# Optimization experiments

Measured on AMD Instinct MI355X. Metric: run time of the kernel, lower is better.

The kernel has to match this reference:

```python
import jax, jax.numpy as jnp
import numpy as np
from jax import lax


def conv2d(x, w, b=None, pad=0, groups=1):
    y = lax.conv_general_dilated(x, w, (1, 1), [(pad, pad), (pad, pad)],
                                 dimension_numbers=('NCHW', 'OIHW', 'NCHW'),
                                 feature_group_count=groups)
    if b is not None:
        y = y + b[None, :, None, None]
    return y


def prelu(x, a):
    return jnp.where(x > 0, x, a * x)


def box_blur(x, k, p):
    # depthwise uniform box filter, groups=3, 'same' output size
    w = jnp.full((3, 1, k, k), 1.0 / (k * k), x.dtype)
    return conv2d(x, w, pad=p, groups=3)


def head(body, hw, hb, c1, c2):
    h = conv2d(body, hw, hb, pad=1)                      # [B,4,H,W]
    g = jnp.mean(h, axis=(2, 3), keepdims=True)          # CALayer: GAP
    s = jax.nn.sigmoid(conv2d(jax.nn.relu(conv2d(g, c1, pad=0)), c2, pad=0))
    return jax.nn.softmax(h * s, axis=1)                 # Softmax2d over channels


def fuse(x, h):
    # kernel_1 is a 1x1 identity conv -> just x
    m2 = box_blur(x, 5, 2)
    m3 = box_blur(x, 15, 7)
    m4 = box_blur(x, 25, 12)
    return h[:, 0:1] * x + h[:, 1:2] * m2 + h[:, 2:3] * m3 + h[:, 3:4] * m4


def setup_inputs() -> dict:
    key = jax.random.key(0)
    ks = jax.random.split(key, 20)
    f32 = jnp.float32
    d = {}
    d['x'] = jax.random.normal(ks[0], (8, 3, 512, 512), f32)
    # body convs
    d['bw1'] = jax.random.normal(ks[1], (32, 3, 3, 3), f32) * 0.05
    d['bb1'] = jnp.zeros((32,), f32)
    d['a1'] = jnp.full((1,), 0.25, f32)
    d['bw2'] = jax.random.normal(ks[2], (64, 32, 3, 3), f32) * 0.05
    d['bb2'] = jnp.zeros((64,), f32)
    d['a2'] = jnp.full((1,), 0.25, f32)
    d['bw3'] = jax.random.normal(ks[3], (32, 64, 3, 3), f32) * 0.05
    d['bb3'] = jnp.zeros((32,), f32)
    d['a3'] = jnp.full((1,), 0.25, f32)
    for i, k0 in zip((1, 2, 3), (4, 8, 12)):
        d[f'h{i}w'] = jax.random.normal(ks[k0], (4, 32, 3, 3), f32) * 0.05
        d[f'h{i}b'] = jnp.zeros((4,), f32)
        d[f'h{i}c1'] = jax.random.normal(ks[k0 + 1], (4, 4, 1, 1), f32) * 0.1
        d[f'h{i}c2'] = jax.random.normal(ks[k0 + 2], (4, 4, 1, 1), f32) * 0.1
    return d


def reference(x, bw1, bb1, a1, bw2, bb2, a2, bw3, bb3, a3,
              h1w, h1b, h1c1, h1c2,
              h2w, h2b, h2c1, h2c2,
              h3w, h3b, h3c1, h3c2):
    body = prelu(conv2d(x, bw1, bb1, pad=1), a1)
    body = prelu(conv2d(body, bw2, bb2, pad=1), a2)
    body = prelu(conv2d(body, bw3, bb3, pad=1), a3)
    h1 = head(body, h1w, h1b, h1c1, h1c2)
    h2 = head(body, h2w, h2b, h2c1, h2c2)
    h3 = head(body, h3w, h3b, h3c1, h3c2)
    out1 = fuse(x, h1)
    out2 = fuse(out1, h2)
    out3 = fuse(out2, h3)
    return out3
```

## Files before the change

### kernel.cpp

```cpp
#include <hip/hip_runtime.h>
#include <math.h>

#define HWSZ (512*512)

typedef unsigned int u32;
typedef __attribute__((ext_vector_type(8))) short short8;
typedef __attribute__((ext_vector_type(4))) float f32x4;

__device__ __forceinline__ unsigned short f2bf(float f) {
    unsigned u = __float_as_uint(f);
    unsigned r = (u + 0x7FFFu + ((u >> 16) & 1u)) >> 16;
    return (unsigned short)r;
}
__device__ __forceinline__ float bf2f(unsigned short h) {
    return __uint_as_float((unsigned)h << 16);
}
__device__ __forceinline__ u32 packhl(float v) {
    unsigned short h = f2bf(v);
    unsigned short l = f2bf(v - bf2f(h));
    return (u32)h | ((u32)l << 16);
}

#define GRAN  3464
#define APLANE (4 * GRAN)

__global__ void prep_weights(const float* __restrict__ w2, const float* __restrict__ w3,
                             const float* __restrict__ hw1, const float* __restrict__ hw2,
                             const float* __restrict__ hw3,
                             const float* __restrict__ hb1, const float* __restrict__ hb2,
                             const float* __restrict__ hb3,
                             unsigned short* __restrict__ w2h, unsigned short* __restrict__ w2l,
                             unsigned short* __restrict__ w3h, unsigned short* __restrict__ w3l,
                             unsigned short* __restrict__ whh, unsigned short* __restrict__ whl,
                             float* __restrict__ hb16)
{
    int i = blockIdx.x * 256 + threadIdx.x;
    if (i < 18432) {
        int tap = i / 2048, r = i % 2048, co = r / 32, ci = r % 32;
        float v = w2[((co * 32 + ci) * 9) + tap];
        unsigned short h = f2bf(v);
        w2h[i] = h; w2l[i] = f2bf(v - bf2f(h));
    } else if (i < 36864) {
        int e = i - 18432;
        int tap = e / 2048, r = e % 2048, co = r / 64, ci = r % 64;
        float v = w3[((co * 64 + ci) * 9) + tap];
        unsigned short h = f2bf(v);
        w3h[e] = h; w3l[e] = f2bf(v - bf2f(h));
    } else if (i < 41472) {
        int e = i - 36864;
        int tap = e / 512, r = e % 512, co16 = r / 32, ci = r % 32;
        float v = 0.f;
        if (co16 < 12) {
            int hd = co16 >> 2, cl = co16 & 3;
            const float* wp = hd == 0 ? hw1 : (hd == 1 ? hw2 : hw3);
            v = wp[((cl * 32 + ci) * 9) + tap];
        }
        unsigned short h = f2bf(v);
        whh[e] = h; whl[e] = f2bf(v - bf2f(h));
    } else if (i < 41488) {
        int j = i - 41472;
        float v = 0.f;
        if (j < 12) {
            const float* bp = (j >> 2) == 0 ? hb1 : ((j >> 2) == 1 ? hb2 : hb3);
            v = bp[j & 3];
        }
        hb16[j] = v;
    }
}

template<int CIN>
__device__ __forceinline__ void stage_tile(const u32* __restrict__ in,
                                           unsigned short* s_a,
                                           int w, int lane, int x1, int y0, int c0)
{
    const int c16 = lane & 15;
    const int g   = lane >> 4;
    for (int it = w; it < 30; it += 4) {
        int r  = it / 5;
        int cb = it % 5;
        int col = cb * 16 + c16;
        if (col < 66) {
            int gy = y0 - 1 + r;
            int gx = x1 - 1 + col;
            u32 d0=0,d1=0,d2=0,d3=0,d4=0,d5=0,d6=0,d7=0;
            if ((unsigned)gy < 512u && (unsigned)gx < 512u) {
                const uint4* p = (const uint4*)(in + ((size_t)(gy * 512 + gx)) * CIN + c0 + g * 8);
                uint4 A = p[0], B = p[1];
                d0=A.x; d1=A.y; d2=A.z; d3=A.w; d4=B.x; d5=B.y; d6=B.z; d7=B.w;
            }
            uint4 hi, lo;
            hi.x = (d0 & 0xffffu) | (d1 << 16);
            hi.y = (d2 & 0xffffu) | (d3 << 16);
            hi.z = (d4 & 0xffffu) | (d5 << 16);
            hi.w = (d6 & 0xffffu) | (d7 << 16);
            lo.x = (d0 >> 16) | (d1 & 0xffff0000u);
            lo.y = (d2 >> 16) | (d3 & 0xffff0000u);
            lo.z = (d4 >> 16) | (d5 & 0xffff0000u);
            lo.w = (d6 >> 16) | (d7 & 0xffff0000u);
            int e = (r * 72 + col) * 8;
            *(uint4*)(s_a + g * GRAN + e) = hi;
            *(uint4*)(s_a + APLANE + g * GRAN + e) = lo;
        }
    }
}

template<int CIN, int COUT>
__global__ __launch_bounds__(256, 2)
void conv_mfma(const u32* __restrict__ in,
               const unsigned short* __restrict__ wh,
               const unsigned short* __restrict__ wl,
               const float* __restrict__ bias,
               const float* __restrict__ alpha,
               u32* __restrict__ out)
{
    constexpr int NTW = COUT / 16;
    __shared__ __align__(16) unsigned short s_a[2 * APLANE];

    const int tid  = threadIdx.x;
    const int w    = tid >> 6;
    const int lane = tid & 63;
    const int ln   = lane & 15;
    const int quad = lane >> 4;
    const int x1   = blockIdx.x * 64;
    const int y0   = blockIdx.y * 4;

    f32x4 acc[4][NTW];
    #pragma unroll
    for (int mt = 0; mt < 4; ++mt)
        #pragma unroll
        for (int nt = 0; nt < NTW; ++nt)
            acc[mt][nt] = (f32x4){0.f, 0.f, 0.f, 0.f};

    for (int c0 = 0; c0 < CIN; c0 += 32) {
        if (c0) __syncthreads();
        stage_tile<CIN>(in, s_a, w, lane, x1, y0, c0);
        __syncthreads();

        #pragma unroll
        for (int tap = 0; tap < 9; ++tap) {
            const int dy = tap / 3, dx = tap % 3;
            short8 bh[NTW], bl[NTW];
            #pragma unroll
            for (int nt = 0; nt < NTW; ++nt) {
                size_t off = ((size_t)(tap * COUT + nt * 16 + ln)) * CIN + c0 + quad * 8;
                bh[nt] = *(const short8*)(wh + off);
                bl[nt] = *(const short8*)(wl + off);
            }
            short8 ah[4], al[4];
            #pragma unroll
            for (int mt = 0; mt < 4; ++mt) {
                const int mti = w * 4 + mt;
                const int rr  = (mti >> 2) + dy;
                const int col = ((mti & 3) << 4) + ln + dx;
                const int off = quad * GRAN + (rr * 72 + col) * 8;
                ah[mt] = *(const short8*)(s_a + off);
                al[mt] = *(const short8*)(s_a + APLANE + off);
            }
            #pragma unroll
            for (int mt = 0; mt < 4; ++mt)
                #pragma unroll
                for (int nt = 0; nt < NTW; ++nt)
                    acc[mt][nt] = __builtin_amdgcn_mfma_f32_16x16x32_bf16(ah[mt], bh[nt], acc[mt][nt], 0, 0, 0);
            #pragma unroll
            for (int mt = 0; mt < 4; ++mt)
                #pragma unroll
                for (int nt = 0; nt < NTW; ++nt)
                    acc[mt][nt] = __builtin_amdgcn_mfma_f32_16x16x32_bf16(al[mt], bh[nt], acc[mt][nt], 0, 0, 0);
            #pragma unroll
            for (int mt = 0; mt < 4; ++mt)
                #pragma unroll
                for (int nt = 0; nt < NTW; ++nt)
                    acc[mt][nt] = __builtin_amdgcn_mfma_f32_16x16x32_bf16(ah[mt], bl[nt], acc[mt][nt], 0, 0, 0);
        }
    }

    const float av = alpha[0];
    float bs[NTW];
    #pragma unroll
    for (int nt = 0; nt < NTW; ++nt) bs[nt] = bias[nt * 16 + ln];
    #pragma unroll
    for (int mt = 0; mt < 4; ++mt) {
        const int mti = w * 4 + mt;
        const int y   = y0 + (mti >> 2);
        const int xb  = x1 + ((mti & 3) << 4) + quad * 4;
        #pragma unroll
        for (int nt = 0; nt < NTW; ++nt) {
            const int co = nt * 16 + ln;
            #pragma unroll
            for (int reg = 0; reg < 4; ++reg) {
                float t = acc[mt][nt][reg] + bs[nt];
                t = t > 0.f ? t : av * t;
                out[((size_t)(y * 512 + xb + reg)) * COUT + co] = packhl(t);
            }
        }
    }
}

__global__ __launch_bounds__(256, 2)
void head_mfma(const u32* __restrict__ in,
               const unsigned short* __restrict__ wh,
               const unsigned short* __restrict__ wl,
               const float* __restrict__ hb,
               float* __restrict__ h, float* __restrict__ g2, int b)
{
    __shared__ __align__(16) unsigned short s_a[2 * APLANE];
    __shared__ float s_red[4][16];

    const int tid  = threadIdx.x;
    const int w    = tid >> 6;
    const int lane = tid & 63;
    const int ln   = lane & 15;
    const int quad = lane >> 4;
    const int x1   = blockIdx.x * 64;
    const int y0   = blockIdx.y * 4;

    f32x4 acc[4];
    #pragma unroll
    for (int mt = 0; mt < 4; ++mt) acc[mt] = (f32x4){0.f, 0.f, 0.f, 0.f};

    stage_tile<32>(in, s_a, w, lane, x1, y0, 0);
    __syncthreads();

    #pragma unroll
    for (int tap = 0; tap < 9; ++tap) {
        const int dy = tap / 3, dx = tap % 3;
        size_t boff = (size_t)tap * 512 + ln * 32 + quad * 8;
        short8 bh = *(const short8*)(wh + boff);
        short8 bl = *(const short8*)(wl + boff);
        short8 ah[4], al[4];
        #pragma unroll
        for (int mt = 0; mt < 4; ++mt) {
            const int mti = w * 4 + mt;
            const int rr  = (mti >> 2) + dy;
            const int col = ((mti & 3) << 4) + ln + dx;
            const int off = quad * GRAN + (rr * 72 + col) * 8;
            ah[mt] = *(const short8*)(s_a + off);
            al[mt] = *(const short8*)(s_a + APLANE + off);
        }
        #pragma unroll
        for (int mt = 0; mt < 4; ++mt)
            acc[mt] = __builtin_amdgcn_mfma_f32_16x16x32_bf16(ah[mt], bh, acc[mt], 0, 0, 0);
        #pragma unroll
        for (int mt = 0; mt < 4; ++mt)
            acc[mt] = __builtin_amdgcn_mfma_f32_16x16x32_bf16(al[mt], bh, acc[mt], 0, 0, 0);
        #pragma unroll
        for (int mt = 0; mt < 4; ++mt)
            acc[mt] = __builtin_amdgcn_mfma_f32_16x16x32_bf16(ah[mt], bl, acc[mt], 0, 0, 0);
    }

    __syncthreads();
    float* s_h = (float*)s_a;
    const float bs = hb[ln];
    float psum = 0.f;
    #pragma unroll
    for (int mt = 0; mt < 4; ++mt) {
        const int mti  = w * 4 + mt;
        const int base = (mti >> 2) * 64 + ((mti & 3) << 4) + quad * 4;
        #pragma unroll
        for (int reg = 0; reg < 4; ++reg) {
            float v = acc[mt][reg] + bs;
            if (ln < 12) s_h[ln * 260 + base + reg] = v;
            psum += v;
        }
    }
    psum += __shfl_down(psum, 16);
    psum += __shfl_down(psum, 32);
    if (lane < 16) s_red[w][lane] = psum;
    __syncthreads();

    if (tid < 192) {
        const int co = tid >> 4, ch = tid & 15;
        const float* src = s_h + co * 260 + ch * 16;
        float4 v0 = *(const float4*)(src);
        float4 v1 = *(const float4*)(src + 4);
        float4 v2 = *(const float4*)(src + 8);
        float4 v3 = *(const float4*)(src + 12);
        const int hd = co >> 2, cl = co & 3;
        float* dst = h + ((size_t)((hd * 8 + b) * 4 + cl)) * HWSZ
                       + (size_t)(y0 + (ch >> 2)) * 512 + x1 + ((ch & 3) << 4);
        *(float4*)(dst)      = v0;
        *(float4*)(dst + 4)  = v1;
        *(float4*)(dst + 8)  = v2;
        *(float4*)(dst + 12) = v3;
    }
    if (tid < 12) {
        float t = s_red[0][tid] + s_red[1][tid] + s_red[2][tid] + s_red[3][tid];
        atomicAdd(&g2[(tid >> 2) * 32 + b * 4 + (tid & 3)], t);
    }
}

__global__ __launch_bounds__(256)
void conv1_nhwc(const float* __restrict__ x, const float* __restrict__ wgt,
                const float* __restrict__ bias, const float* __restrict__ alpha,
                u32* __restrict__ out)
{
    __shared__ float s_in[3][6][72];
    __shared__ float s_w[3][9][32];
    __shared__ float s_b[32];
    const int tid = threadIdx.x;
    const int x1 = blockIdx.x * 64, y0 = blockIdx.y * 4;

    for (int i = tid; i < 3 * 6 * 66; i += 256) {
        int ci = i / 396, rm = i % 396;
        int r = rm / 66, cc = rm % 66;
        int gy = y0 - 1 + r, gx = x1 - 1 + cc;
        float v = 0.f;
        if ((unsigned)gy < 512u && (unsigned)gx < 512u)
            v = x[(size_t)ci * HWSZ + gy * 512 + gx];
        s_in[ci][r][cc] = v;
    }
    for (int i = tid; i < 864; i += 256) {
        int co = i & 31, rm = i >> 5;
        int ci = rm / 9, tap = rm % 9;
        s_w[ci][tap][co] = wgt[(co * 3 + ci) * 9 + tap];
    }
    if (tid < 32) s_b[tid] = bias[tid];
    __syncthreads();

    const int ty = tid >> 6, tx = tid & 63;
    float acc[32];
    #pragma unroll
    for (int i = 0; i < 32; ++i) acc[i] = 0.f;
    #pragma unroll
    for (int ci = 0; ci < 3; ++ci)
        #pragma unroll
        for (int tap = 0; tap < 9; ++tap) {
            const int dy = tap / 3, dx = tap % 3;
            float iv = s_in[ci][ty + dy][tx + dx];
            #pragma unroll
            for (int c4 = 0; c4 < 8; ++c4) {
                float4 wv = *(const float4*)&s_w[ci][tap][c4 * 4];
                acc[c4*4+0] = fmaf(iv, wv.x, acc[c4*4+0]);
                acc[c4*4+1] = fmaf(iv, wv.y, acc[c4*4+1]);
                acc[c4*4+2] = fmaf(iv, wv.z, acc[c4*4+2]);
                acc[c4*4+3] = fmaf(iv, wv.w, acc[c4*4+3]);
            }
        }
    const float av = alpha[0];
    u32* o = out + ((size_t)((y0 + ty) * 512 + x1 + tx)) * 32;
    #pragma unroll
    for (int c4 = 0; c4 < 8; ++c4) {
        uint4 pk;
        float t;
        t = acc[c4*4+0] + s_b[c4*4+0]; t = t > 0.f ? t : av * t; pk.x = packhl(t);
        t = acc[c4*4+1] + s_b[c4*4+1]; t = t > 0.f ? t : av * t; pk.y = packhl(t);
        t = acc[c4*4+2] + s_b[c4*4+2]; t = t > 0.f ? t : av * t; pk.z = packhl(t);
        t = acc[c4*4+3] + s_b[c4*4+3]; t = t > 0.f ? t : av * t; pk.w = packhl(t);
        *(uint4*)(o + c4 * 4) = pk;
    }
}

__global__ void zero_k(float* p, int n)
{
    int i = blockIdx.x * 256 + threadIdx.x;
    if (i < n) p[i] = 0.f;
}

__global__ void ca_kernel(const float* __restrict__ g,
                          const float* __restrict__ c11, const float* __restrict__ c12,
                          const float* __restrict__ c21, const float* __restrict__ c22,
                          const float* __restrict__ c31, const float* __restrict__ c32,
                          float* __restrict__ sOut)
{
    int t = threadIdx.x;
    if (t >= 24) return;
    int head = t / 8, b = t % 8;
    const float* c1 = head == 0 ? c11 : (head == 1 ? c21 : c31);
    const float* c2 = head == 0 ? c12 : (head == 1 ? c22 : c32);
    float m[4], v[4];
    #pragma unroll
    for (int i = 0; i < 4; ++i) m[i] = g[head * 32 + b * 4 + i] * (1.0f / 262144.0f);
    #pragma unroll
    for (int j = 0; j < 4; ++j) {
        float xv = c1[j*4+0]*m[0] + c1[j*4+1]*m[1] + c1[j*4+2]*m[2] + c1[j*4+3]*m[3];
        v[j] = fmaxf(xv, 0.f);
    }
    #pragma unroll
    for (int j = 0; j < 4; ++j) {
        float xv = c2[j*4+0]*v[0] + c2[j*4+1]*v[1] + c2[j*4+2]*v[2] + c2[j*4+3]*v[3];
        sOut[head * 32 + b * 4 + j] = 1.f / (1.f + __expf(-xv));
    }
}

__global__ __launch_bounds__(256)
void sat_row(const float* __restrict__ src, float* __restrict__ S)
{
    const int y  = blockIdx.x;
    const int bc = blockIdx.y;
    float* Sp = S + (size_t)bc * 263169;
    const int tid = threadIdx.x;
    if (y == 0) {
        for (int i = tid; i < 513; i += 256) Sp[i] = 0.f;
        return;
    }
    const float2* row2 = (const float2*)(src + (size_t)bc * HWSZ + (size_t)(y - 1) * 512);
    float2 ab = row2[tid];
    float ps = ab.x + ab.y;
    float v = ps;
    const int lane = tid & 63;
    #pragma unroll
    for (int off = 1; off < 64; off <<= 1) {
        float u = __shfl_up(v, off);
        if (lane >= off) v += u;
    }
    __shared__ float wsum[4];
    const int wv = tid >> 6;
    if (lane == 63) wsum[wv] = v;
    __syncthreads();
    float woff = 0.f;
    #pragma unroll
    for (int k = 0; k < 4; ++k) if (k < wv) woff += wsum[k];
    float excl = woff + v - ps;
    float* o = Sp + (size_t)y * 513;
    if (tid == 0) o[0] = 0.f;
    o[1 + 2 * tid] = excl + ab.x;
    o[2 + 2 * tid] = excl + ab.x + ab.y;
}

__global__ __launch_bounds__(256)
void sat_col(float* __restrict__ S)
{
    const int bc = blockIdx.x;
    const int c  = 1 + blockIdx.y * 256 + threadIdx.x;
    float* P = S + (size_t)bc * 263169 + c;
    float run = 0.f;
    for (int r0 = 1; r0 <= 512; r0 += 16) {
        float v[16];
        #pragma unroll
        for (int i = 0; i < 16; ++i) v[i] = P[(size_t)(r0 + i) * 513];
        #pragma unroll
        for (int i = 0; i < 16; ++i) { run += v[i]; v[i] = run; }
        #pragma unroll
        for (int i = 0; i < 16; ++i) P[(size_t)(r0 + i) * 513] = v[i];
    }
}

__device__ __forceinline__ float boxsum(const float* __restrict__ S, int y, int x, int p)
{
    int y0 = max(y - p, 0), x0 = max(x - p, 0);
    int y1 = min(y + p, 511) + 1, x1 = min(x + p, 511) + 1;
    return S[y1 * 513 + x1] - S[y0 * 513 + x1] - S[y1 * 513 + x0] + S[y0 * 513 + x0];
}

__global__ __launch_bounds__(256)
void fuse_kernel(const float* __restrict__ cur, const float* __restrict__ h,
                 const float* __restrict__ sv, const float* __restrict__ S,
                 float* __restrict__ out, int head)
{
    const int idx = blockIdx.x * 256 + threadIdx.x;
    const int b   = idx >> 18;
    const int rem = idx & 262143;
    const int y   = rem >> 9;
    const int x   = rem & 511;

    const float* sp = sv + head * 32 + b * 4;
    const float* hp = h + (size_t)((head * 8 + b) * 4) * HWSZ + rem;
    float z0 = hp[0]          * sp[0];
    float z1 = hp[HWSZ]       * sp[1];
    float z2 = hp[2 * HWSZ]   * sp[2];
    float z3 = hp[3 * HWSZ]   * sp[3];
    float m  = fmaxf(fmaxf(z0, z1), fmaxf(z2, z3));
    float e0 = __expf(z0 - m), e1 = __expf(z1 - m), e2 = __expf(z2 - m), e3 = __expf(z3 - m);
    float inv = 1.f / (e0 + e1 + e2 + e3);
    float p0 = e0 * inv, p1 = e1 * inv, p2 = e2 * inv, p3 = e3 * inv;

    #pragma unroll
    for (int c = 0; c < 3; ++c) {
        const float* Sp = S + (size_t)(b * 3 + c) * 263169;
        float xv = cur[((size_t)b * 3 + c) * HWSZ + rem];
        float m2 = boxsum(Sp, y, x, 2)  * (1.f / 25.f);
        float m3 = boxsum(Sp, y, x, 7)  * (1.f / 225.f);
        float m4 = boxsum(Sp, y, x, 12) * (1.f / 625.f);
        out[((size_t)b * 3 + c) * HWSZ + rem] = p0 * xv + p1 * m2 + p2 * m3 + p3 * m4;
    }
}

extern "C" void kernel_launch(void* const* d_in, const int* in_sizes, int n_in,
                              void* d_out, int out_size, void* d_ws, size_t ws_size,
                              hipStream_t stream)
{
    (void)in_sizes; (void)n_in; (void)out_size; (void)ws_size;
    const float* x    = (const float*)d_in[0];
    const float* bw1  = (const float*)d_in[1];
    const float* bb1  = (const float*)d_in[2];
    const float* a1   = (const float*)d_in[3];
    const float* bw2  = (const float*)d_in[4];
    const float* bb2  = (const float*)d_in[5];
    const float* a2   = (const float*)d_in[6];
    const float* bw3  = (const float*)d_in[7];
    const float* bb3  = (const float*)d_in[8];
    const float* a3   = (const float*)d_in[9];
    const float* h1w  = (const float*)d_in[10];
    const float* h1b  = (const float*)d_in[11];
    const float* h1c1 = (const float*)d_in[12];
    const float* h1c2 = (const float*)d_in[13];
    const float* h2w  = (const float*)d_in[14];
    const float* h2b  = (const float*)d_in[15];
    const float* h2c1 = (const float*)d_in[16];
    const float* h2c2 = (const float*)d_in[17];
    const float* h3w  = (const float*)d_in[18];
    const float* h3b  = (const float*)d_in[19];
    const float* h3c1 = (const float*)d_in[20];
    const float* h3c2 = (const float*)d_in[21];

    float* ws   = (float*)d_ws;
    u32*   t1u  = (u32*)ws;
    u32*   t2u  = t1u + 8388608;
    float* hbuf = (float*)(t2u + 16777216);
    float* gbuf = hbuf + 25165824;
    float* sbuf = gbuf + 96;
    unsigned short* wb = (unsigned short*)(sbuf + 96);
    unsigned short* w2h = wb;
    unsigned short* w2l = wb + 18432;
    unsigned short* w3h = wb + 36864;
    unsigned short* w3l = wb + 55296;
    unsigned short* whh = wb + 73728;
    unsigned short* whl = wb + 78336;
    float* hb16 = (float*)(wb + 82944);
    float* SAT  = (float*)t2u;
    float* ping = (float*)t1u;

    dim3 blk(256);

    prep_weights<<<dim3(163), blk, 0, stream>>>(bw2, bw3, h1w, h2w, h3w,
                                                h1b, h2b, h3b,
                                                w2h, w2l, w3h, w3l, whh, whl, hb16);
    zero_k<<<dim3(1), dim3(128), 0, stream>>>(gbuf, 96);

    for (int b = 0; b < 8; ++b) {
        conv1_nhwc<<<dim3(8, 128), blk, 0, stream>>>(x + (size_t)b * 3 * HWSZ,
                                                     bw1, bb1, a1, t1u);
        conv_mfma<32, 64><<<dim3(8, 128), blk, 0, stream>>>(t1u, w2h, w2l, bb2, a2, t2u);
        conv_mfma<64, 32><<<dim3(8, 128), blk, 0, stream>>>(t2u, w3h, w3l, bb3, a3, t1u);
        head_mfma<<<dim3(8, 128), blk, 0, stream>>>(t1u, whh, whl, hb16, hbuf, gbuf, b);
    }

    ca_kernel<<<dim3(1), dim3(64), 0, stream>>>(gbuf, h1c1, h1c2, h2c1, h2c2,
                                                h3c1, h3c2, sbuf);

    const float* cur = x;
    for (int i = 0; i < 3; ++i) {
        sat_row<<<dim3(513, 24), blk, 0, stream>>>(cur, SAT);
        sat_col<<<dim3(24, 2), blk, 0, stream>>>(SAT);
        float* nxt = (i == 2) ? (float*)d_out : ping;
        fuse_kernel<<<dim3(8192), blk, 0, stream>>>(cur, hbuf, sbuf, SAT, nxt, i);
        cur = nxt;
    }
}
```

Baseline: 1.423 ms.

## Stage conv tiles via direct global-to-LDS DMA from padded split hi/lo planes

Activations are now stored as separate bf16 hi and lo planes in a zero-bordered, padded NHWC layout (pitch 516), in place of interleaved hi/lo u32 words. With that layout, tile staging for the MFMA convs and the head conv can use global_load_lds 16-byte DMA straight into LDS, with no per-thread bounds checks or hi/lo unpacking in registers. A one-time border-zeroing kernel keeps the halo valid across batches. The trade-off is larger workspace and scalar 16-bit output stores in the conv epilogue, which may coalesce less well than the previous packed writes.

```diff
diff --git a/kernel.cpp b/kernel.cpp
--- a/kernel.cpp
+++ b/kernel.cpp
@@ -15,14 +15,18 @@
 __device__ __forceinline__ float bf2f(unsigned short h) {
     return __uint_as_float((unsigned)h << 16);
 }
-__device__ __forceinline__ u32 packhl(float v) {
-    unsigned short h = f2bf(v);
-    unsigned short l = f2bf(v - bf2f(h));
-    return (u32)h | ((u32)l << 16);
-}
-
-#define GRAN  3464
-#define APLANE (4 * GRAN)
+
+#define PITCH 516
+#define PROWS 514
+#define LDSPLANE 15360
+
+__device__ __forceinline__ void dma16(const unsigned short* g, unsigned short* l)
+{
+    __builtin_amdgcn_global_load_lds(
+        (const __attribute__((address_space(1))) unsigned int*)g,
+        (__attribute__((address_space(3))) unsigned int*)l,
+        16, 0, 0);
+}
 
 __global__ void prep_weights(const float* __restrict__ w2, const float* __restrict__ w3,
                              const float* __restrict__ hw1, const float* __restrict__ hw2,
@@ -68,53 +72,69 @@
     }
 }
 
+__global__ void zero_border(unsigned short* __restrict__ ph,
+                            unsigned short* __restrict__ pl, int logc)
+{
+    int i = blockIdx.x * 256 + threadIdx.x;
+    const int C = 1 << logc;
+    if (i >= 3080 * C) return;
+    int pix = i >> logc, ch = i & (C - 1);
+    int row, col;
+    if (pix < 2 * PITCH) {
+        row = (pix < PITCH) ? 0 : (PROWS - 1);
+        col = (pix < PITCH) ? pix : pix - PITCH;
+    } else {
+        int q = pix - 2 * PITCH;
+        row = 1 + (q >> 2);
+        int c = q & 3;
+        col = (c == 0) ? 0 : 512 + c;
+    }
+    size_t o = ((size_t)(row * PITCH + col)) * C + ch;
+    ph[o] = 0;
+    pl[o] = 0;
+}
+
+template<int CIN, int RB>
+__device__ __forceinline__ void stage_half(const unsigned short* bp, unsigned short* ldsb)
+{
+    #pragma unroll
+    for (int k = 0; k < 15; ++k) {
+        const int rid = RB + k;
+        const int r = rid / 5, cb = rid % 5;
+        dma16(bp + (size_t)(r * PITCH + cb * 16) * CIN, ldsb + rid * 512);
+    }
+}
+
 template<int CIN>
-__device__ __forceinline__ void stage_tile(const u32* __restrict__ in,
-                                           unsigned short* s_a,
-                                           int w, int lane, int x1, int y0, int c0)
+__device__ __forceinline__ void stage_dma(const unsigned short* __restrict__ inh,
+                                          const unsigned short* __restrict__ inl,
+                                          unsigned short* s_a,
+                                          int w, int lane, int x1, int y0, int c0)
 {
     const int c16 = lane & 15;
     const int g   = lane >> 4;
-    for (int it = w; it < 30; it += 4) {
-        int r  = it / 5;
-        int cb = it % 5;
-        int col = cb * 16 + c16;
-        if (col < 66) {
-            int gy = y0 - 1 + r;
-            int gx = x1 - 1 + col;
-            u32 d0=0,d1=0,d2=0,d3=0,d4=0,d5=0,d6=0,d7=0;
-            if ((unsigned)gy < 512u && (unsigned)gx < 512u) {
-                const uint4* p = (const uint4*)(in + ((size_t)(gy * 512 + gx)) * CIN + c0 + g * 8);
-                uint4 A = p[0], B = p[1];
-                d0=A.x; d1=A.y; d2=A.z; d3=A.w; d4=B.x; d5=B.y; d6=B.z; d7=B.w;
-            }
-            uint4 hi, lo;
-            hi.x = (d0 & 0xffffu) | (d1 << 16);
-            hi.y = (d2 & 0xffffu) | (d3 << 16);
-            hi.z = (d4 & 0xffffu) | (d5 << 16);
-            hi.w = (d6 & 0xffffu) | (d7 << 16);
-            lo.x = (d0 >> 16) | (d1 & 0xffff0000u);
-            lo.y = (d2 >> 16) | (d3 & 0xffff0000u);
-            lo.z = (d4 >> 16) | (d5 & 0xffff0000u);
-            lo.w = (d6 >> 16) | (d7 & 0xffff0000u);
-            int e = (r * 72 + col) * 8;
-            *(uint4*)(s_a + g * GRAN + e) = hi;
-            *(uint4*)(s_a + APLANE + g * GRAN + e) = lo;
-        }
-    }
+    const unsigned short* base = (w < 2) ? inh : inl;
+    unsigned short* ldsb = s_a + ((w < 2) ? 0 : LDSPLANE);
+    const unsigned short* bp = base
+        + ((size_t)(y0 * PITCH + x1 + c16)) * CIN + c0 + g * 8;
+    if (w & 1) stage_half<CIN, 15>(bp, ldsb);
+    else       stage_half<CIN, 0>(bp, ldsb);
+}
+
+__device__ __forceinline__ int frag_off(int rr, int col, int quad)
+{
+    return ((rr * 5 + (col >> 4)) << 9) + (((quad << 4) | (col & 15)) << 3);
 }
 
 template<int CIN, int COUT>
 __global__ __launch_bounds__(256, 2)
-void conv_mfma(const u32* __restrict__ in,
-               const unsigned short* __restrict__ wh,
-               const unsigned short* __restrict__ wl,
-               const float* __restrict__ bias,
-               const float* __restrict__ alpha,
-               u32* __restrict__ out)
+void conv_mfma(const unsigned short* __restrict__ inh, const unsigned short* __restrict__ inl,
+               const unsigned short* __restrict__ wh, const unsigned short* __restrict__ wl,
+               const float* __restrict__ bias, const float* __restrict__ alpha,
+               unsigned short* __restrict__ outh, unsigned short* __restrict__ outl)
 {
     constexpr int NTW = COUT / 16;
-    __shared__ __align__(16) unsigned short s_a[2 * APLANE];
+    __shared__ __align__(16) unsigned short s_a[2 * LDSPLANE];
 
     const int tid  = threadIdx.x;
     const int w    = tid >> 6;
@@ -133,7 +153,8 @@
 
     for (int c0 = 0; c0 < CIN; c0 += 32) {
         if (c0) __syncthreads();
-        stage_tile<CIN>(in, s_a, w, lane, x1, y0, c0);
+        stage_dma<CIN>(inh, inl, s_a, w, lane, x1, y0, c0);
+        asm volatile("s_waitcnt vmcnt(0)" ::: "memory");
         __syncthreads();
 
         #pragma unroll
@@ -152,9 +173,9 @@
                 const int mti = w * 4 + mt;
                 const int rr  = (mti >> 2) + dy;
                 const int col = ((mti & 3) << 4) + ln + dx;
-                const int off = quad * GRAN + (rr * 72 + col) * 8;
+                const int off = frag_off(rr, col, quad);
                 ah[mt] = *(const short8*)(s_a + off);
-                al[mt] = *(const short8*)(s_a + APLANE + off);
+                al[mt] = *(const short8*)(s_a + LDSPLANE + off);
             }
             #pragma unroll
             for (int mt = 0; mt < 4; ++mt)
@@ -190,20 +211,23 @@
             for (int reg = 0; reg < 4; ++reg) {
                 float t = acc[mt][nt][reg] + bs[nt];
                 t = t > 0.f ? t : av * t;
-                out[((size_t)(y * 512 + xb + reg)) * COUT + co] = packhl(t);
+                unsigned short hh = f2bf(t);
+                unsigned short ll = f2bf(t - bf2f(hh));
+                size_t o = ((size_t)((y + 1) * PITCH + xb + reg + 1)) * COUT + co;
+                outh[o] = hh;
+                outl[o] = ll;
             }
         }
     }
 }
 
 __global__ __launch_bounds__(256, 2)
-void head_mfma(const u32* __restrict__ in,
-               const unsigned short* __restrict__ wh,
-               const unsigned short* __restrict__ wl,
+void head_mfma(const unsigned short* __restrict__ inh, const unsigned short* __restrict__ inl,
+               const unsigned short* __restrict__ wh, const unsigned short* __restrict__ wl,
                const float* __restrict__ hb,
                float* __restrict__ h, float* __restrict__ g2, int b)
 {
-    __shared__ __align__(16) unsigned short s_a[2 * APLANE];
+    __shared__ __align__(16) unsigned short s_a[2 * LDSPLANE];
     __shared__ float s_red[4][16];
 
     const int tid  = threadIdx.x;
@@ -218,7 +242,8 @@
     #pragma unroll
     for (int mt = 0; mt < 4; ++mt) acc[mt] = (f32x4){0.f, 0.f, 0.f, 0.f};
 
-    stage_tile<32>(in, s_a, w, lane, x1, y0, 0);
+    stage_dma<32>(inh, inl, s_a, w, lane, x1, y0, 0);
+    asm volatile("s_waitcnt vmcnt(0)" ::: "memory");
     __syncthreads();
 
     #pragma unroll
@@ -233,9 +258,9 @@
             const int mti = w * 4 + mt;
             const int rr  = (mti >> 2) + dy;
             const int col = ((mti & 3) << 4) + ln + dx;
-            const int off = quad * GRAN + (rr * 72 + col) * 8;
+            const int off = frag_off(rr, col, quad);
             ah[mt] = *(const short8*)(s_a + off);
-            al[mt] = *(const short8*)(s_a + APLANE + off);
+            al[mt] = *(const short8*)(s_a + LDSPLANE + off);
         }
         #pragma unroll
         for (int mt = 0; mt < 4; ++mt)
@@ -292,7 +317,7 @@
 __global__ __launch_bounds__(256)
 void conv1_nhwc(const float* __restrict__ x, const float* __restrict__ wgt,
                 const float* __restrict__ bias, const float* __restrict__ alpha,
-                u32* __restrict__ out)
+                unsigned short* __restrict__ outh, unsigned short* __restrict__ outl)
 {
     __shared__ float s_in[3][6][72];
     __shared__ float s_w[3][9][32];
@@ -337,16 +362,21 @@
             }
         }
     const float av = alpha[0];
-    u32* o = out + ((size_t)((y0 + ty) * 512 + x1 + tx)) * 32;
-    #pragma unroll
-    for (int c4 = 0; c4 < 8; ++c4) {
-        uint4 pk;
-        float t;
-        t = acc[c4*4+0] + s_b[c4*4+0]; t = t > 0.f ? t : av * t; pk.x = packhl(t);
-        t = acc[c4*4+1] + s_b[c4*4+1]; t = t > 0.f ? t : av * t; pk.y = packhl(t);
-        t = acc[c4*4+2] + s_b[c4*4+2]; t = t > 0.f ? t : av * t; pk.z = packhl(t);
-        t = acc[c4*4+3] + s_b[c4*4+3]; t = t > 0.f ? t : av * t; pk.w = packhl(t);
-        *(uint4*)(o + c4 * 4) = pk;
+    u32 ph[16], pl[16];
+    #pragma unroll
+    for (int cp = 0; cp < 16; ++cp) {
+        float t0 = acc[2*cp]     + s_b[2*cp];     t0 = t0 > 0.f ? t0 : av * t0;
+        float t1 = acc[2*cp + 1] + s_b[2*cp + 1]; t1 = t1 > 0.f ? t1 : av * t1;
+        unsigned short h0 = f2bf(t0), h1 = f2bf(t1);
+        unsigned short l0 = f2bf(t0 - bf2f(h0)), l1 = f2bf(t1 - bf2f(h1));
+        ph[cp] = (u32)h0 | ((u32)h1 << 16);
+        pl[cp] = (u32)l0 | ((u32)l1 << 16);
+    }
+    size_t o = ((size_t)((y0 + ty + 1) * PITCH + x1 + tx + 1)) * 32;
+    #pragma unroll
+    for (int q = 0; q < 4; ++q) {
+        *(uint4*)(outh + o + q * 8) = (uint4){ph[4*q], ph[4*q+1], ph[4*q+2], ph[4*q+3]};
+        *(uint4*)(outl + o + q * 8) = (uint4){pl[4*q], pl[4*q+1], pl[4*q+2], pl[4*q+3]};
     }
 }
 
@@ -503,10 +533,14 @@
     const float* h3c1 = (const float*)d_in[20];
     const float* h3c2 = (const float*)d_in[21];
 
-    float* ws   = (float*)d_ws;
-    u32*   t1u  = (u32*)ws;
-    u32*   t2u  = t1u + 8388608;
-    float* hbuf = (float*)(t2u + 16777216);
+    const size_t T1P = (size_t)PROWS * PITCH * 32;
+    const size_t T2P = (size_t)PROWS * PITCH * 64;
+
+    unsigned short* t1h = (unsigned short*)d_ws;
+    unsigned short* t1l = t1h + T1P;
+    unsigned short* t2h = t1l + T1P;
+    unsigned short* t2l = t2h + T2P;
+    float* hbuf = (float*)(t2l + T2P);
     float* gbuf = hbuf + 25165824;
     float* sbuf = gbuf + 96;
     unsigned short* wb = (unsigned short*)(sbuf + 96);
@@ -517,8 +551,8 @@
     unsigned short* whh = wb + 73728;
     unsigned short* whl = wb + 78336;
     float* hb16 = (float*)(wb + 82944);
-    float* SAT  = (float*)t2u;
-    float* ping = (float*)t1u;
+    float* SAT  = (float*)t2h;
+    float* ping = (float*)t1h;
 
     dim3 blk(256);
 
@@ -526,13 +560,15 @@
                                                 h1b, h2b, h3b,
                                                 w2h, w2l, w3h, w3l, whh, whl, hb16);
     zero_k<<<dim3(1), dim3(128), 0, stream>>>(gbuf, 96);
+    zero_border<<<dim3(385), blk, 0, stream>>>(t1h, t1l, 5);
+    zero_border<<<dim3(770), blk, 0, stream>>>(t2h, t2l, 6);
 
     for (int b = 0; b < 8; ++b) {
         conv1_nhwc<<<dim3(8, 128), blk, 0, stream>>>(x + (size_t)b * 3 * HWSZ,
-                                                     bw1, bb1, a1, t1u);
-        conv_mfma<32, 64><<<dim3(8, 128), blk, 0, stream>>>(t1u, w2h, w2l, bb2, a2, t2u);
-        conv_mfma<64, 32><<<dim3(8, 128), blk, 0, stream>>>(t2u, w3h, w3l, bb3, a3, t1u);
-        head_mfma<<<dim3(8, 128), blk, 0, stream>>>(t1u, whh, whl, hb16, hbuf, gbuf, b);
+                                                     bw1, bb1, a1, t1h, t1l);
+        conv_mfma<32, 64><<<dim3(8, 128), blk, 0, stream>>>(t1h, t1l, w2h, w2l, bb2, a2, t2h, t2l);
+        conv_mfma<64, 32><<<dim3(8, 128), blk, 0, stream>>>(t2h, t2l, w3h, w3l, bb3, a3, t1h, t1l);
+        head_mfma<<<dim3(8, 128), blk, 0, stream>>>(t1h, t1l, whh, whl, hb16, hbuf, gbuf, b);
     }
 
     ca_kernel<<<dim3(1), dim3(64), 0, stream>>>(gbuf, h1c1, h1c2, h2c1, h2c2,
```

Result: slower. 1.515 ms (+6.5%).

## Batch multiple images per body-conv launch when workspace permits

Applied to the files above, without the earlier changes.

The body conv kernels now treat several batch images as one tall image by extending grid.y and deriving the batch index from the row. Intermediate buffers are sized by a group factor G picked from the available workspace, so up to all 8 images run in one launch per stage. This cuts launch count and tail effects from small grids (1024 blocks), at the cost of much larger intermediate buffers and lower cache locality. conv_mfma's stage_tile is changed to clamp padding at image boundaries within the stacked layout.

```diff
diff --git a/kernel.cpp b/kernel.cpp
--- a/kernel.cpp
+++ b/kernel.cpp
@@ -75,15 +75,17 @@
 {
     const int c16 = lane & 15;
     const int g   = lane >> 4;
+    const int yb  = y0 - (y0 & 511);
     for (int it = w; it < 30; it += 4) {
         int r  = it / 5;
         int cb = it % 5;
         int col = cb * 16 + c16;
         if (col < 66) {
-            int gy = y0 - 1 + r;
+            int yl = (y0 & 511) - 1 + r;
             int gx = x1 - 1 + col;
             u32 d0=0,d1=0,d2=0,d3=0,d4=0,d5=0,d6=0,d7=0;
-            if ((unsigned)gy < 512u && (unsigned)gx < 512u) {
+            if ((unsigned)yl < 512u && (unsigned)gx < 512u) {
+                const int gy = yb + yl;
                 const uint4* p = (const uint4*)(in + ((size_t)(gy * 512 + gx)) * CIN + c0 + g * 8);
                 uint4 A = p[0], B = p[1];
                 d0=A.x; d1=A.y; d2=A.z; d3=A.w; d4=B.x; d5=B.y; d6=B.z; d7=B.w;
@@ -201,7 +203,7 @@
                const unsigned short* __restrict__ wh,
                const unsigned short* __restrict__ wl,
                const float* __restrict__ hb,
-               float* __restrict__ h, float* __restrict__ g2, int b)
+               float* __restrict__ h, float* __restrict__ g2, int b0)
 {
     __shared__ __align__(16) unsigned short s_a[2 * APLANE];
     __shared__ float s_red[4][16];
@@ -213,6 +215,8 @@
     const int quad = lane >> 4;
     const int x1   = blockIdx.x * 64;
     const int y0   = blockIdx.y * 4;
+    const int b    = b0 + (y0 >> 9);
+    const int yl0  = y0 & 511;
 
     f32x4 acc[4];
     #pragma unroll
@@ -277,7 +281,7 @@
         float4 v3 = *(const float4*)(src + 12);
         const int hd = co >> 2, cl = co & 3;
         float* dst = h + ((size_t)((hd * 8 + b) * 4 + cl)) * HWSZ
-                       + (size_t)(y0 + (ch >> 2)) * 512 + x1 + ((ch & 3) << 4);
+                       + (size_t)(yl0 + (ch >> 2)) * 512 + x1 + ((ch & 3) << 4);
         *(float4*)(dst)      = v0;
         *(float4*)(dst + 4)  = v1;
         *(float4*)(dst + 8)  = v2;
@@ -299,14 +303,15 @@
     __shared__ float s_b[32];
     const int tid = threadIdx.x;
     const int x1 = blockIdx.x * 64, y0 = blockIdx.y * 4;
+    const int b = y0 >> 9, yb0 = y0 & 511;
 
     for (int i = tid; i < 3 * 6 * 66; i += 256) {
         int ci = i / 396, rm = i % 396;
         int r = rm / 66, cc = rm % 66;
-        int gy = y0 - 1 + r, gx = x1 - 1 + cc;
+        int yl = yb0 - 1 + r, gx = x1 - 1 + cc;
         float v = 0.f;
-        if ((unsigned)gy < 512u && (unsigned)gx < 512u)
-            v = x[(size_t)ci * HWSZ + gy * 512 + gx];
+        if ((unsigned)yl < 512u && (unsigned)gx < 512u)
+            v = x[((size_t)(b * 3 + ci)) * HWSZ + yl * 512 + gx];
         s_in[ci][r][cc] = v;
     }
     for (int i = tid; i < 864; i += 256) {
@@ -479,7 +484,7 @@
                               void* d_out, int out_size, void* d_ws, size_t ws_size,
                               hipStream_t stream)
 {
-    (void)in_sizes; (void)n_in; (void)out_size; (void)ws_size;
+    (void)in_sizes; (void)n_in; (void)out_size;
     const float* x    = (const float*)d_in[0];
     const float* bw1  = (const float*)d_in[1];
     const float* bb1  = (const float*)d_in[2];
@@ -503,10 +508,17 @@
     const float* h3c1 = (const float*)d_in[20];
     const float* h3c2 = (const float*)d_in[21];
 
+    int G = 1;
+    for (int g = 8; g > 1; g >>= 1) {
+        size_t need = ((size_t)g * 25165824 + 25166016) * 4
+                    + 82944 * 2 + 64 + 256;
+        if (ws_size >= need) { G = g; break; }
+    }
+
     float* ws   = (float*)d_ws;
     u32*   t1u  = (u32*)ws;
-    u32*   t2u  = t1u + 8388608;
-    float* hbuf = (float*)(t2u + 16777216);
+    u32*   t2u  = t1u + (size_t)G * 8388608;
+    float* hbuf = (float*)(t2u + (size_t)G * 16777216);
     float* gbuf = hbuf + 25165824;
     float* sbuf = gbuf + 96;
     unsigned short* wb = (unsigned short*)(sbuf + 96);
@@ -527,12 +539,13 @@
                                                 w2h, w2l, w3h, w3l, whh, whl, hb16);
     zero_k<<<dim3(1), dim3(128), 0, stream>>>(gbuf, 96);
 
-    for (int b = 0; b < 8; ++b) {
-        conv1_nhwc<<<dim3(8, 128), blk, 0, stream>>>(x + (size_t)b * 3 * HWSZ,
-                                                     bw1, bb1, a1, t1u);
-        conv_mfma<32, 64><<<dim3(8, 128), blk, 0, stream>>>(t1u, w2h, w2l, bb2, a2, t2u);
-        conv_mfma<64, 32><<<dim3(8, 128), blk, 0, stream>>>(t2u, w3h, w3l, bb3, a3, t1u);
-        head_mfma<<<dim3(8, 128), blk, 0, stream>>>(t1u, whh, whl, hb16, hbuf, gbuf, b);
+    const dim3 bodyGrid(8, 128 * G);
+    for (int g = 0; g < 8; g += G) {
+        conv1_nhwc<<<bodyGrid, blk, 0, stream>>>(x + (size_t)g * 3 * HWSZ,
+                                                 bw1, bb1, a1, t1u);
+        conv_mfma<32, 64><<<bodyGrid, blk, 0, stream>>>(t1u, w2h, w2l, bb2, a2, t2u);
+        conv_mfma<64, 32><<<bodyGrid, blk, 0, stream>>>(t2u, w3h, w3l, bb3, a3, t1u);
+        head_mfma<<<bodyGrid, blk, 0, stream>>>(t1u, whh, whl, hb16, hbuf, gbuf, g);
     }
 
     ca_kernel<<<dim3(1), dim3(64), 0, stream>>>(gbuf, h1c1, h1c2, h2c1, h2c2,
```

Result: no change. 1.426 ms (+0.2%).
